# Kernel optimization log

Hardware: AMD Instinct MI355X
Metric: run time of the kernel (lower is better)

Reference implementation:

```python
import jax, jax.numpy as jnp
import numpy as np

B, T_PRIOR, N_FEAT = 8192, 168, 11
DEC_FEAT, HID, T_DEC = 7, 64, 48

def setup_inputs() -> dict:
    key = jax.random.key(0)
    ks = jax.random.split(key, 12)
    s = 1.0 / np.sqrt(HID)
    def u(k, shape):
        return jax.random.uniform(k, shape, jnp.float32, -s, s)
    return {
        "prior": jax.random.normal(ks[0], (B, T_PRIOR, N_FEAT), jnp.float32),
        "teacher_seq": jax.random.normal(ks[1], (B, T_DEC, DEC_FEAT), jnp.float32),
        "enc_Wih": u(ks[2], (3 * HID, N_FEAT)),
        "enc_Whh": u(ks[3], (3 * HID, HID)),
        "enc_bih": u(ks[4], (3 * HID,)),
        "enc_bhh": u(ks[5], (3 * HID,)),
        "dec_Wih": u(ks[6], (3 * HID, DEC_FEAT)),
        "dec_Whh": u(ks[7], (3 * HID, HID)),
        "dec_bih": u(ks[8], (3 * HID,)),
        "dec_bhh": u(ks[9], (3 * HID,)),
        "fc_W": u(ks[10], (1, HID)),
        "fc_b": u(ks[11], (1,)),
    }

def _gru_cell(x, h, Wih, Whh, bih, bhh):
    # PyTorch GRU gate math, gate order (r, z, n)
    gi = x @ Wih.T + bih            # [B, 3H]
    gh = h @ Whh.T + bhh            # [B, 3H]
    i_r, i_z, i_n = jnp.split(gi, 3, axis=-1)
    h_r, h_z, h_n = jnp.split(gh, 3, axis=-1)
    r = jax.nn.sigmoid(i_r + h_r)
    z = jax.nn.sigmoid(i_z + h_z)
    n = jnp.tanh(i_n + r * h_n)
    return (1.0 - z) * n + z * h

def reference(prior, teacher_seq, enc_Wih, enc_Whh, enc_bih, enc_bhh,
              dec_Wih, dec_Whh, dec_bih, dec_bhh, fc_W, fc_b):
    Bsz = prior.shape[0]
    h0 = jnp.zeros((Bsz, HID), prior.dtype)

    # ---- encoder: run GRU over prior, keep final hidden state ----
    def enc_step(h, x_t):
        return _gru_cell(x_t, h, enc_Wih, enc_Whh, enc_bih, enc_bhh), None
    h_enc, _ = jax.lax.scan(enc_step, h0, jnp.swapaxes(prior, 0, 1))

    # teacher features for step i+1, padded with zeros for the unused last step
    tn = jnp.concatenate(
        [teacher_seq[:, 1:, :], jnp.zeros_like(teacher_seq[:, :1, :])], axis=1)

    def dec_step(carry, tn_t):
        h, x = carry
        h = _gru_cell(x, h, dec_Wih, dec_Whh, dec_bih, dec_bhh)
        pred = h @ fc_W.T + fc_b                      # [B, 1]
        next_x = jnp.concatenate(
            [tn_t[:, 0:4], pred, tn_t[:, 5:7]], axis=-1)  # [B, 7]
        return (h, next_x), pred

    x0 = teacher_seq[:, 0, 0:7]
    (_, _), preds = jax.lax.scan(dec_step, (h_enc, x0), jnp.swapaxes(tn, 0, 1))
    # preds: [T_DEC, B, 1] -> [B, T_DEC]
    return jnp.swapaxes(preds[:, :, 0], 0, 1)
```

## Files before the change

kernel.cpp:

```cpp
#include <hip/hip_runtime.h>
#include <hip/hip_bf16.h>

#define T_PRIOR 168
#define N_FEAT 11
#define DEC_FEAT 7
#define T_DEC 48
#define BATCH 8192
#define XROWU 136
#define ROWB (XROWU*2)
#define BUFB (16*ROWB)

typedef __attribute__((ext_vector_type(8))) short short8;
typedef __attribute__((ext_vector_type(4))) float f32x4;
typedef __attribute__((ext_vector_type(4))) int i32x4;

#define MFMA __builtin_amdgcn_mfma_f32_16x16x32_bf16
#define L2E 1.4426950408889634f

static __device__ __forceinline__ unsigned fbits(float f){union{float f;unsigned u;}v;v.f=f;return v.u;}
static __device__ __forceinline__ unsigned short bf16rne(float f){
    unsigned x=fbits(f);
    return (unsigned short)((x+0x7fffu+((x>>16)&1u))>>16);
}
static __device__ __forceinline__ float sigm2(float xs){
    return __builtin_amdgcn_rcpf(1.0f + __builtin_amdgcn_exp2f(-xs));
}
static __device__ __forceinline__ float tanh2(float ys){
    return fmaf(2.0f, __builtin_amdgcn_rcpf(1.0f + __builtin_amdgcn_exp2f(-ys)), -1.0f);
}
static __device__ __forceinline__ short8 s8(i32x4 v){union{i32x4 i;short8 s;}q;q.i=v;return q.s;}
static __device__ __forceinline__ unsigned pk2bf(float a, float b){
    __hip_bfloat162 p = __float22bfloat162_rn(make_float2(a, b));
    union { __hip_bfloat162 h; unsigned u; } cv; cv.h = p; return cv.u;
}

__global__ __launch_bounds__(256) __attribute__((amdgpu_waves_per_eu(2,2)))
void gru_mfma(const float* __restrict__ prior, const float* __restrict__ teacher,
              const float* __restrict__ eWih, const float* __restrict__ eWhh,
              const float* __restrict__ eBih, const float* __restrict__ eBhh,
              const float* __restrict__ dWih, const float* __restrict__ dWhh,
              const float* __restrict__ dBih, const float* __restrict__ dBhh,
              const float* __restrict__ fcW, const float* __restrict__ fcB,
              float* __restrict__ out)
{
    __shared__ __align__(16) unsigned short sH[2][1024];
    __shared__ __align__(16) unsigned short sX[2*16*XROWU];
    __shared__ __align__(16) float sPartial[2][16][4];

    const int tid  = (int)threadIdx.x;
    const int lane = tid & 63;
    const int u    = tid >> 6;
    const int c    = lane & 15;
    const int g    = lane >> 4;
    const int row0 = (int)blockIdx.x * 16;

    const unsigned cs = ((unsigned)(c & 7)) << 4;
    const unsigned rbA0 = (unsigned)(c*128) + (((unsigned)(g*16)) ^ cs);
    const unsigned rbA1 = (unsigned)(c*128) + (((unsigned)(64 + g*16)) ^ cs);
    unsigned pubOff[4];
#pragma unroll
    for (int q = 0; q < 4; ++q) {
        int r = g*4 + q;
        pubOff[q] = (unsigned)(r*128) + (((unsigned)(32*u + 2*c)) ^ (((unsigned)(r&7))<<4));
    }

    const unsigned xRowB = (unsigned)(c*ROWB);
    const unsigned xE_off = (g < 2) ? (unsigned)(g*16) : 256u;
    const unsigned xE_mul = (g < 2) ? 32u : 0u;
    const unsigned xD_off = (g == 0) ? 0u : 256u;
    const unsigned xD_mul = (g == 0) ? 32u : 0u;
    char* sXB = (char*)sX;

    const int srow = tid >> 4, sli = tid & 15;
    char* sXwr = sXB + srow*ROWB;
    int offE[6], offD[4];
#pragma unroll
    for (int n = 0; n < 6; ++n) { int k = sli + 16*n; offE[n] = ((k/11)*16 + (k%11))*2; }
#pragma unroll
    for (int n = 0; n < 4; ++n) { int k = sli + 16*n; offD[n] = ((k/7)*16 + (k%7))*2; }
    const float* gP = prior   + (size_t)(row0 + srow)*(T_PRIOR*N_FEAT) + sli;
    const float* gT = teacher + (size_t)(row0 + srow)*(T_DEC*DEC_FEAT) + sli;

    short8 BHH[3][2], BIH[3];
    f32x4 bR4, bZ4, bH4, bI4;
    auto loadPhase = [&](const float* Wih, const float* Whh,
                         const float* bih, const float* bhh, int kvalid) {
        const int rwb = u*16 + c;
#pragma unroll
        for (int gate = 0; gate < 3; ++gate) {
            const float gs = (gate == 2) ? (2.0f*L2E) : L2E;
            const int rw = gate*64 + rwb;
#pragma unroll
            for (int kt = 0; kt < 2; ++kt) {
                union { short8 v; unsigned short s[8]; } fh;
#pragma unroll
                for (int j = 0; j < 8; ++j) {
                    int kap = kt*32 + g*8 + j;
                    fh.s[j] = bf16rne(Whh[rw*64 + kap] * gs);
                }
                BHH[gate][kt] = fh.v;
            }
            union { short8 v; unsigned short s[8]; } fi;
#pragma unroll
            for (int j = 0; j < 8; ++j) {
                int k = g*8 + j;
                fi.s[j] = (k < kvalid) ? bf16rne(Wih[rw*kvalid + k] * gs) : (unsigned short)0;
            }
            BIH[gate] = fi.v;
        }
        const int un = u*16 + c;
        float vR = (bih[un] + bhh[un]) * L2E;
        float vZ = (bih[64+un] + bhh[64+un]) * L2E;
        float vI = bih[128+un] * (2.0f*L2E);
        float vH = bhh[128+un] * (2.0f*L2E);
        bR4 = (f32x4){vR,vR,vR,vR};
        bZ4 = (f32x4){vZ,vZ,vZ,vZ};
        bH4 = (f32x4){vH,vH,vH,vH};
        bI4 = (f32x4){vI,vI,vI,vI};
    };

    float h[4] = {0.0f, 0.0f, 0.0f, 0.0f};

    auto gates_publish = [&](int p, f32x4 R, f32x4 Z, f32x4 Hh, f32x4 I) {
        char* hw = (char*)&sH[p^1][0];
        float hn[4];
#pragma unroll
        for (int q = 0; q < 4; ++q) {
            float rr = sigm2(R[q]);
            float zz = sigm2(Z[q]);
            float nn = tanh2(fmaf(rr, Hh[q], I[q]));
            hn[q] = nn + zz*(h[q] - nn);
            h[q] = hn[q];
        }
        unsigned w01 = pk2bf(hn[0], hn[1]);
        unsigned w23 = pk2bf(hn[2], hn[3]);
        *(unsigned short*)(hw + pubOff[0]) = (unsigned short)(w01 & 0xffffu);
        *(unsigned short*)(hw + pubOff[1]) = (unsigned short)(w01 >> 16);
        *(unsigned short*)(hw + pubOff[2]) = (unsigned short)(w23 & 0xffffu);
        *(unsigned short*)(hw + pubOff[3]) = (unsigned short)(w23 >> 16);
    };

    f32x4 xR, xZ, xI;
    auto xpart = [&](short8 xf) {
        xR = MFMA(xf, BIH[0], bR4, 0,0,0);
        xZ = MFMA(xf, BIH[1], bZ4, 0,0,0);
        xI = MFMA(xf, BIH[2], bI4, 0,0,0);
    };

    auto hh_step = [&](int p) {
        const char* hb = (const char*)&sH[p][0];
        short8 a0 = *(const short8*)(hb + rbA0);
        short8 a1 = *(const short8*)(hb + rbA1);
        __builtin_amdgcn_s_setprio(1);
        f32x4 R = MFMA(a0, BHH[0][0], xR, 0,0,0);
        R = MFMA(a1, BHH[0][1], R, 0,0,0);
        f32x4 Z = MFMA(a0, BHH[1][0], xZ, 0,0,0);
        Z = MFMA(a1, BHH[1][1], Z, 0,0,0);
        f32x4 Hh = MFMA(a0, BHH[2][0], bH4, 0,0,0);
        Hh = MFMA(a1, BHH[2][1], Hh, 0,0,0);
        __builtin_amdgcn_s_setprio(0);
        gates_publish(p, R, Z, Hh, xI);
    };

    auto gru_step = [&](int p, short8 xf) {
        const char* hb = (const char*)&sH[p][0];
        short8 a0 = *(const short8*)(hb + rbA0);
        short8 a1 = *(const short8*)(hb + rbA1);
        f32x4 R = MFMA(a0, BHH[0][0], bR4, 0,0,0);
        R = MFMA(a1, BHH[0][1], R, 0,0,0);
        R = MFMA(xf, BIH[0],    R, 0,0,0);
        f32x4 Z = MFMA(a0, BHH[1][0], bZ4, 0,0,0);
        Z = MFMA(a1, BHH[1][1], Z, 0,0,0);
        Z = MFMA(xf, BIH[1],    Z, 0,0,0);
        f32x4 Hh = MFMA(a0, BHH[2][0], bH4, 0,0,0);
        Hh = MFMA(a1, BHH[2][1], Hh, 0,0,0);
        f32x4 I = MFMA(xf, BIH[2], bI4, 0,0,0);
        gates_publish(p, R, Z, Hh, I);
    };

    {
        unsigned* z0 = (unsigned*)&sH[0][0];
#pragma unroll
        for (int it = 0; it < 2; ++it) z0[tid + 256*it] = 0u;
    }
#pragma unroll
    for (int it = 0; it < 6; ++it) {
        int e = tid + 256*it;
        int b = e / 768, rem = e % 768;
        int idx;
        if (rem < 640) {
            int r = rem / 40, q2 = rem % 40;
            idx = b*(16*XROWU) + r*XROWU + (q2/5)*16 + 11 + q2%5;
        } else {
            int rem2 = rem - 640;
            idx = b*(16*XROWU) + (rem2 >> 3)*XROWU + 128 + (rem2 & 7);
        }
        sX[idx] = 0;
    }
    loadPhase(eWih, eWhh, eBih, eBhh, N_FEAT);
    {
        float sv[6];
#pragma unroll
        for (int n = 0; n < 5; ++n) sv[n] = gP[16*n];
        sv[5] = (sli < 8) ? gP[80] : 0.0f;
#pragma unroll
        for (int n = 0; n < 5; ++n) *(unsigned short*)(sXwr + offE[n]) = bf16rne(sv[n]);
        if (sli < 8) *(unsigned short*)(sXwr + offE[5]) = bf16rne(sv[5]);
    }
    __syncthreads();
    {
        short8 xf0 = *(const short8*)(sXB + (xRowB + xE_off));
        xpart(xf0);
    }

    for (int ch = 0; ch < 21; ++ch) {
        const unsigned wbo = (unsigned)(((ch + 1) & 1) * BUFB);
        const bool st = (ch < 20);
        float sv[6];
#pragma unroll
        for (int s = 0; s < 8; ++s) {
            const int t = ch*8 + s;
            __syncthreads();
            if (s == 0 && st) {
                const float* sp = gP + 88*(ch+1);
#pragma unroll
                for (int n = 0; n < 5; ++n) sv[n] = sp[16*n];
                sv[5] = (sli < 8) ? sp[80] : 0.0f;
            }
            hh_step(t & 1);
            if (s == 1 && st) {
#pragma unroll
                for (int n = 0; n < 5; ++n) *(unsigned short*)(sXwr + wbo + offE[n]) = bf16rne(sv[n]);
                if (sli < 8) *(unsigned short*)(sXwr + wbo + offE[5]) = bf16rne(sv[5]);
            }
            if (t < T_PRIOR - 1) {
                const int tn = t + 1;
                const unsigned nbo = (unsigned)(((tn >> 3) & 1) * BUFB);
                short8 xf = *(const short8*)(sXB + (nbo + xRowB + xE_off + (unsigned)(tn & 7)*xE_mul));
                xpart(xf);
            }
        }
    }

    __syncthreads();
    loadPhase(dWih, dWhh, dBih, dBhh, DEC_FEAT);
    const float fwc = fcW[u*16 + c];
    const float fb  = fcB[0];
#pragma unroll
    for (int it = 0; it < 9; ++it) {
        int e = tid + 256*it;
        int b = e / 1152, rem = e % 1152;
        int r = rem / 72, q2 = rem % 72;
        sX[b*(16*XROWU) + r*XROWU + (q2/9)*16 + 7 + q2%9] = 0;
    }
    {
        float sv[4];
#pragma unroll
        for (int n = 0; n < 3; ++n) sv[n] = gT[16*n];
        sv[3] = (sli < 8) ? gT[48] : 0.0f;
#pragma unroll
        for (int n = 0; n < 3; ++n) *(unsigned short*)(sXwr + offD[n]) = bf16rne(sv[n]);
        if (sli < 8) *(unsigned short*)(sXwr + offD[3]) = bf16rne(sv[3]);
    }

    for (int ch = 0; ch < 6; ++ch) {
        const unsigned bo  = (unsigned)((ch & 1) * BUFB);
        const unsigned wbo = (unsigned)(((ch + 1) & 1) * BUFB);
        const bool st = (ch < 5);
        float sv[4];
#pragma unroll
        for (int s = 0; s < 8; ++s) {
            const int i = ch*8 + s;
            __syncthreads();
            if (s == 0 && st) {
                const float* sp = gT + 56*(ch+1);
#pragma unroll
                for (int n = 0; n < 3; ++n) sv[n] = sp[16*n];
                sv[3] = (sli < 8) ? sp[48] : 0.0f;
            }
            const bool hasPred = (s > 0) || (ch > 0);
            i32x4 xi = *(const i32x4*)(sXB + (bo + xRowB + xD_off + (unsigned)s*xD_mul));
            if (hasPred) {
                f32x4 pp = *(const f32x4*)&sPartial[(s & 1) ^ 1][c][0];
                float pred = pp[0] + pp[1] + pp[2] + pp[3] + fb;
                if (g == 0)
                    xi[2] = (int)(((unsigned)xi[2] & 0xffff0000u) | (unsigned)bf16rne(pred));
                if (u == 0 && g == 0)
                    out[(size_t)(row0 + c)*T_DEC + (i - 1)] = pred;
            }
            gru_step(s & 1, s8(xi));
#pragma unroll
            for (int q = 0; q < 4; ++q) {
                float v = h[q] * fwc;
                v += __shfl_xor(v, 1, 64);
                v += __shfl_xor(v, 2, 64);
                v += __shfl_xor(v, 4, 64);
                v += __shfl_xor(v, 8, 64);
                if (c == 0) sPartial[s & 1][g*4 + q][u] = v;
            }
            if (s == 1 && st) {
#pragma unroll
                for (int n = 0; n < 3; ++n) *(unsigned short*)(sXwr + wbo + offD[n]) = bf16rne(sv[n]);
                if (sli < 8) *(unsigned short*)(sXwr + wbo + offD[3]) = bf16rne(sv[3]);
            }
        }
    }
    __syncthreads();
    if (u == 0 && g == 0) {
        f32x4 pp = *(const f32x4*)&sPartial[1][c][0];
        float pred = pp[0] + pp[1] + pp[2] + pp[3] + fb;
        out[(size_t)(row0 + c)*T_DEC + (T_DEC - 1)] = pred;
    }
}

extern "C" void kernel_launch(void* const* d_in, const int* in_sizes, int n_in,
                              void* d_out, int out_size, void* d_ws, size_t ws_size,
                              hipStream_t stream)
{
    const float* prior   = (const float*)d_in[0];
    const float* teacher = (const float*)d_in[1];
    const float* eWih    = (const float*)d_in[2];
    const float* eWhh    = (const float*)d_in[3];
    const float* eBih    = (const float*)d_in[4];
    const float* eBhh    = (const float*)d_in[5];
    const float* dWih    = (const float*)d_in[6];
    const float* dWhh    = (const float*)d_in[7];
    const float* dBih    = (const float*)d_in[8];
    const float* dBhh    = (const float*)d_in[9];
    const float* fcW     = (const float*)d_in[10];
    const float* fcB     = (const float*)d_in[11];
    float* out = (float*)d_out;

    dim3 grid(BATCH / 16);
    dim3 block(256);
    hipLaunchKernelGGL(gru_mfma, grid, block, 0, stream,
                       prior, teacher, eWih, eWhh, eBih, eBhh,
                       dWih, dWhh, dBih, dBhh, fcW, fcB, out);
}
```

Before: 142.6 us.

## Split GRU hidden-state K dimension across two wave groups with LDS exchange

Doubles the block to 512 threads and splits the 64-wide hidden reduction (K) between two wave groups. Each group computes half of the Whh MFMAs and half the input projections, then exchanges partial accumulators through shared memory so each group finishes gate math for half the rows. This shortens the serial per-step MFMA chain and spreads the gate math across more waves. In exchange it adds a second barrier per timestep, LDS exchange traffic, and a single hidden buffer instead of a double buffer.

Result: slower. 511.0 us (+258.3%).

```diff
diff --git a/kernel.cpp b/kernel.cpp
--- a/kernel.cpp
+++ b/kernel.cpp
@@ -12,6 +12,7 @@
 
 typedef __attribute__((ext_vector_type(8))) short short8;
 typedef __attribute__((ext_vector_type(4))) float f32x4;
+typedef __attribute__((ext_vector_type(2))) float f32x2;
 typedef __attribute__((ext_vector_type(4))) int i32x4;
 
 #define MFMA __builtin_amdgcn_mfma_f32_16x16x32_bf16
@@ -34,33 +35,35 @@
     union { __hip_bfloat162 h; unsigned u; } cv; cv.h = p; return cv.u;
 }
 
-__global__ __launch_bounds__(256) __attribute__((amdgpu_waves_per_eu(2,2)))
-void gru_mfma(const float* __restrict__ prior, const float* __restrict__ teacher,
-              const float* __restrict__ eWih, const float* __restrict__ eWhh,
-              const float* __restrict__ eBih, const float* __restrict__ eBhh,
-              const float* __restrict__ dWih, const float* __restrict__ dWhh,
-              const float* __restrict__ dBih, const float* __restrict__ dBhh,
-              const float* __restrict__ fcW, const float* __restrict__ fcB,
-              float* __restrict__ out)
+__global__ __launch_bounds__(512)
+void gru_ks(const float* __restrict__ prior, const float* __restrict__ teacher,
+            const float* __restrict__ eWih, const float* __restrict__ eWhh,
+            const float* __restrict__ eBih, const float* __restrict__ eBhh,
+            const float* __restrict__ dWih, const float* __restrict__ dWhh,
+            const float* __restrict__ dBih, const float* __restrict__ dBhh,
+            const float* __restrict__ fcW, const float* __restrict__ fcB,
+            float* __restrict__ out)
 {
-    __shared__ __align__(16) unsigned short sH[2][1024];
+    __shared__ __align__(16) unsigned short sH[1024];
+    __shared__ __align__(16) float sXch[2][4][4][128];
     __shared__ __align__(16) unsigned short sX[2*16*XROWU];
     __shared__ __align__(16) float sPartial[2][16][4];
 
     const int tid  = (int)threadIdx.x;
     const int lane = tid & 63;
-    const int u    = tid >> 6;
+    const int w    = tid >> 6;
+    const int u    = w & 3;
+    const int sW   = __builtin_amdgcn_readfirstlane(w >> 2);
     const int c    = lane & 15;
     const int g    = lane >> 4;
     const int row0 = (int)blockIdx.x * 16;
 
     const unsigned cs = ((unsigned)(c & 7)) << 4;
-    const unsigned rbA0 = (unsigned)(c*128) + (((unsigned)(g*16)) ^ cs);
-    const unsigned rbA1 = (unsigned)(c*128) + (((unsigned)(64 + g*16)) ^ cs);
-    unsigned pubOff[4];
-#pragma unroll
-    for (int q = 0; q < 4; ++q) {
-        int r = g*4 + q;
+    const unsigned rbA = (unsigned)(c*128) + (((unsigned)(sW*64 + g*16)) ^ cs);
+    unsigned pubOff[2];
+#pragma unroll
+    for (int q = 0; q < 2; ++q) {
+        int r = g*4 + sW*2 + q;
         pubOff[q] = (unsigned)(r*128) + (((unsigned)(32*u + 2*c)) ^ (((unsigned)(r&7))<<4));
     }
 
@@ -71,7 +74,11 @@
     const unsigned xD_mul = (g == 0) ? 32u : 0u;
     char* sXB = (char*)sX;
 
-    const int srow = tid >> 4, sli = tid & 15;
+    float* xw = &sXch[sW][u][0][0] + lane*2;
+    const float* xr = &sXch[sW^1][u][0][0] + lane*2;
+
+    const bool stager = (tid < 256);
+    const int srow = (tid & 255) >> 4, sli = tid & 15;
     char* sXwr = sXB + srow*ROWB;
     int offE[6], offD[4];
 #pragma unroll
@@ -81,111 +88,135 @@
     const float* gP = prior   + (size_t)(row0 + srow)*(T_PRIOR*N_FEAT) + sli;
     const float* gT = teacher + (size_t)(row0 + srow)*(T_DEC*DEC_FEAT) + sli;
 
-    short8 BHH[3][2], BIH[3];
-    f32x4 bR4, bZ4, bH4, bI4;
+    short8 BHH[3];
+    short8 BIx[2];
+    float bR, bZ, bH, bI;
     auto loadPhase = [&](const float* Wih, const float* Whh,
-                         const float* bih, const float* bhh, int kvalid) {
+                         const float* bih, const float* bhh, int kv) {
         const int rwb = u*16 + c;
 #pragma unroll
         for (int gate = 0; gate < 3; ++gate) {
             const float gs = (gate == 2) ? (2.0f*L2E) : L2E;
             const int rw = gate*64 + rwb;
-#pragma unroll
-            for (int kt = 0; kt < 2; ++kt) {
-                union { short8 v; unsigned short s[8]; } fh;
-#pragma unroll
-                for (int j = 0; j < 8; ++j) {
-                    int kap = kt*32 + g*8 + j;
-                    fh.s[j] = bf16rne(Whh[rw*64 + kap] * gs);
-                }
-                BHH[gate][kt] = fh.v;
-            }
+            union { short8 v; unsigned short s[8]; } fh;
+#pragma unroll
+            for (int j = 0; j < 8; ++j)
+                fh.s[j] = bf16rne(Whh[rw*64 + sW*32 + g*8 + j] * gs);
+            BHH[gate] = fh.v;
+        }
+        auto mkBI = [&](int gate) -> short8 {
+            const float gs = (gate == 2) ? (2.0f*L2E) : L2E;
+            const int rw = gate*64 + rwb;
             union { short8 v; unsigned short s[8]; } fi;
 #pragma unroll
             for (int j = 0; j < 8; ++j) {
                 int k = g*8 + j;
-                fi.s[j] = (k < kvalid) ? bf16rne(Wih[rw*kvalid + k] * gs) : (unsigned short)0;
-            }
-            BIH[gate] = fi.v;
-        }
+                fi.s[j] = (k < kv) ? bf16rne(Wih[rw*kv + k] * gs) : (unsigned short)0;
+            }
+            return fi.v;
+        };
+        if (sW == 0) { BIx[0] = mkBI(2); }
+        else         { BIx[0] = mkBI(0); BIx[1] = mkBI(1); }
         const int un = u*16 + c;
-        float vR = (bih[un] + bhh[un]) * L2E;
-        float vZ = (bih[64+un] + bhh[64+un]) * L2E;
-        float vI = bih[128+un] * (2.0f*L2E);
-        float vH = bhh[128+un] * (2.0f*L2E);
-        bR4 = (f32x4){vR,vR,vR,vR};
-        bZ4 = (f32x4){vZ,vZ,vZ,vZ};
-        bH4 = (f32x4){vH,vH,vH,vH};
-        bI4 = (f32x4){vI,vI,vI,vI};
-    };
-
-    float h[4] = {0.0f, 0.0f, 0.0f, 0.0f};
-
-    auto gates_publish = [&](int p, f32x4 R, f32x4 Z, f32x4 Hh, f32x4 I) {
-        char* hw = (char*)&sH[p^1][0];
-        float hn[4];
-#pragma unroll
-        for (int q = 0; q < 4; ++q) {
-            float rr = sigm2(R[q]);
-            float zz = sigm2(Z[q]);
-            float nn = tanh2(fmaf(rr, Hh[q], I[q]));
-            hn[q] = nn + zz*(h[q] - nn);
-            h[q] = hn[q];
-        }
-        unsigned w01 = pk2bf(hn[0], hn[1]);
-        unsigned w23 = pk2bf(hn[2], hn[3]);
-        *(unsigned short*)(hw + pubOff[0]) = (unsigned short)(w01 & 0xffffu);
-        *(unsigned short*)(hw + pubOff[1]) = (unsigned short)(w01 >> 16);
-        *(unsigned short*)(hw + pubOff[2]) = (unsigned short)(w23 & 0xffffu);
-        *(unsigned short*)(hw + pubOff[3]) = (unsigned short)(w23 >> 16);
-    };
-
-    f32x4 xR, xZ, xI;
-    auto xpart = [&](short8 xf) {
-        xR = MFMA(xf, BIH[0], bR4, 0,0,0);
-        xZ = MFMA(xf, BIH[1], bZ4, 0,0,0);
-        xI = MFMA(xf, BIH[2], bI4, 0,0,0);
-    };
-
-    auto hh_step = [&](int p) {
-        const char* hb = (const char*)&sH[p][0];
-        short8 a0 = *(const short8*)(hb + rbA0);
-        short8 a1 = *(const short8*)(hb + rbA1);
+        bR = (bih[un] + bhh[un]) * L2E;
+        bZ = (bih[64+un] + bhh[64+un]) * L2E;
+        bI = bih[128+un] * (2.0f*L2E);
+        bH = bhh[128+un] * (2.0f*L2E);
+    };
+
+    const f32x4 z4 = (f32x4){0.0f, 0.0f, 0.0f, 0.0f};
+    f32x4 xpR, xpZ, xpI;
+    f32x4 aR, aZ, aH, aI;
+    float h0 = 0.0f, h1 = 0.0f;
+    float fwc = 0.0f, fb = 0.0f;
+
+    auto xpartE = [&](short8 xf) {
+        if (sW == 0) { xpI = MFMA(xf, BIx[0], z4, 0,0,0); }
+        else         { xpR = MFMA(xf, BIx[0], z4, 0,0,0);
+                       xpZ = MFMA(xf, BIx[1], z4, 0,0,0); }
+    };
+
+    auto xch_write = [&]() {
+        if (sW == 0) {
+            *(f32x2*)(xw +   0) = (f32x2){aR[2], aR[3]};
+            *(f32x2*)(xw + 128) = (f32x2){aZ[2], aZ[3]};
+            *(f32x2*)(xw + 256) = (f32x2){aH[2], aH[3]};
+            *(f32x2*)(xw + 384) = (f32x2){aI[2], aI[3]};
+        } else {
+            *(f32x2*)(xw +   0) = (f32x2){aR[0], aR[1]};
+            *(f32x2*)(xw + 128) = (f32x2){aZ[0], aZ[1]};
+            *(f32x2*)(xw + 256) = (f32x2){aH[0], aH[1]};
+        }
+    };
+
+    auto phase1E = [&]() {
+        short8 a = *(const short8*)((const char*)sH + rbA);
         __builtin_amdgcn_s_setprio(1);
-        f32x4 R = MFMA(a0, BHH[0][0], xR, 0,0,0);
-        R = MFMA(a1, BHH[0][1], R, 0,0,0);
-        f32x4 Z = MFMA(a0, BHH[1][0], xZ, 0,0,0);
-        Z = MFMA(a1, BHH[1][1], Z, 0,0,0);
-        f32x4 Hh = MFMA(a0, BHH[2][0], bH4, 0,0,0);
-        Hh = MFMA(a1, BHH[2][1], Hh, 0,0,0);
+        if (sW == 0) {
+            aR = MFMA(a, BHH[0], z4, 0,0,0);
+            aZ = MFMA(a, BHH[1], z4, 0,0,0);
+            aH = MFMA(a, BHH[2], z4, 0,0,0);
+            aI = xpI;
+        } else {
+            aR = MFMA(a, BHH[0], xpR, 0,0,0);
+            aZ = MFMA(a, BHH[1], xpZ, 0,0,0);
+            aH = MFMA(a, BHH[2], z4, 0,0,0);
+        }
         __builtin_amdgcn_s_setprio(0);
-        gates_publish(p, R, Z, Hh, xI);
-    };
-
-    auto gru_step = [&](int p, short8 xf) {
-        const char* hb = (const char*)&sH[p][0];
-        short8 a0 = *(const short8*)(hb + rbA0);
-        short8 a1 = *(const short8*)(hb + rbA1);
-        f32x4 R = MFMA(a0, BHH[0][0], bR4, 0,0,0);
-        R = MFMA(a1, BHH[0][1], R, 0,0,0);
-        R = MFMA(xf, BIH[0],    R, 0,0,0);
-        f32x4 Z = MFMA(a0, BHH[1][0], bZ4, 0,0,0);
-        Z = MFMA(a1, BHH[1][1], Z, 0,0,0);
-        Z = MFMA(xf, BIH[1],    Z, 0,0,0);
-        f32x4 Hh = MFMA(a0, BHH[2][0], bH4, 0,0,0);
-        Hh = MFMA(a1, BHH[2][1], Hh, 0,0,0);
-        f32x4 I = MFMA(xf, BIH[2], bI4, 0,0,0);
-        gates_publish(p, R, Z, Hh, I);
-    };
-
-    {
-        unsigned* z0 = (unsigned*)&sH[0][0];
-#pragma unroll
-        for (int it = 0; it < 2; ++it) z0[tid + 256*it] = 0u;
-    }
-#pragma unroll
-    for (int it = 0; it < 6; ++it) {
-        int e = tid + 256*it;
+        xch_write();
+    };
+
+    auto phase1D = [&](short8 xf) {
+        short8 a = *(const short8*)((const char*)sH + rbA);
+        __builtin_amdgcn_s_setprio(1);
+        if (sW == 0) {
+            aR = MFMA(a, BHH[0], z4, 0,0,0);
+            aZ = MFMA(a, BHH[1], z4, 0,0,0);
+            aH = MFMA(a, BHH[2], z4, 0,0,0);
+            aI = MFMA(xf, BIx[0], z4, 0,0,0);
+        } else {
+            aR = MFMA(a, BHH[0], z4, 0,0,0);
+            aR = MFMA(xf, BIx[0], aR, 0,0,0);
+            aZ = MFMA(a, BHH[1], z4, 0,0,0);
+            aZ = MFMA(xf, BIx[1], aZ, 0,0,0);
+            aH = MFMA(a, BHH[2], z4, 0,0,0);
+        }
+        __builtin_amdgcn_s_setprio(0);
+        xch_write();
+    };
+
+    auto phase2 = [&]() {
+        f32x2 pR = *(const f32x2*)(xr +   0);
+        f32x2 pZ = *(const f32x2*)(xr + 128);
+        f32x2 pH = *(const f32x2*)(xr + 256);
+        float Rt0, Rt1, Zt0, Zt1, Ht0, Ht1, It0, It1;
+        if (sW == 0) {
+            Rt0 = aR[0]+pR[0]+bR; Rt1 = aR[1]+pR[1]+bR;
+            Zt0 = aZ[0]+pZ[0]+bZ; Zt1 = aZ[1]+pZ[1]+bZ;
+            Ht0 = aH[0]+pH[0]+bH; Ht1 = aH[1]+pH[1]+bH;
+            It0 = aI[0]+bI;       It1 = aI[1]+bI;
+        } else {
+            f32x2 pI = *(const f32x2*)(xr + 384);
+            Rt0 = aR[2]+pR[0]+bR; Rt1 = aR[3]+pR[1]+bR;
+            Zt0 = aZ[2]+pZ[0]+bZ; Zt1 = aZ[3]+pZ[1]+bZ;
+            Ht0 = aH[2]+pH[0]+bH; Ht1 = aH[3]+pH[1]+bH;
+            It0 = pI[0]+bI;       It1 = pI[1]+bI;
+        }
+        float rr0 = sigm2(Rt0), zz0 = sigm2(Zt0);
+        float nn0 = tanh2(fmaf(rr0, Ht0, It0));
+        h0 = nn0 + zz0*(h0 - nn0);
+        float rr1 = sigm2(Rt1), zz1 = sigm2(Zt1);
+        float nn1 = tanh2(fmaf(rr1, Ht1, It1));
+        h1 = nn1 + zz1*(h1 - nn1);
+        unsigned w01 = pk2bf(h0, h1);
+        *(unsigned short*)((char*)sH + pubOff[0]) = (unsigned short)(w01 & 0xffffu);
+        *(unsigned short*)((char*)sH + pubOff[1]) = (unsigned short)(w01 >> 16);
+    };
+
+    if (tid < 512) ((unsigned*)sH)[tid] = 0u;
+#pragma unroll
+    for (int it = 0; it < 3; ++it) {
+        int e = tid + 512*it;
         int b = e / 768, rem = e % 768;
         int idx;
         if (rem < 640) {
@@ -198,7 +229,7 @@
         sX[idx] = 0;
     }
     loadPhase(eWih, eWhh, eBih, eBhh, N_FEAT);
-    {
+    if (stager) {
         float sv[6];
 #pragma unroll
         for (int n = 0; n < 5; ++n) sv[n] = gP[16*n];
@@ -210,7 +241,7 @@
     __syncthreads();
     {
         short8 xf0 = *(const short8*)(sXB + (xRowB + xE_off));
-        xpart(xf0);
+        xpartE(xf0);
     }
 
     for (int ch = 0; ch < 21; ++ch) {
@@ -221,14 +252,16 @@
         for (int s = 0; s < 8; ++s) {
             const int t = ch*8 + s;
             __syncthreads();
-            if (s == 0 && st) {
+            if (s == 0 && st && stager) {
                 const float* sp = gP + 88*(ch+1);
 #pragma unroll
                 for (int n = 0; n < 5; ++n) sv[n] = sp[16*n];
                 sv[5] = (sli < 8) ? sp[80] : 0.0f;
             }
-            hh_step(t & 1);
-            if (s == 1 && st) {
+            phase1E();
+            __syncthreads();
+            phase2();
+            if (s == 1 && st && stager) {
 #pragma unroll
                 for (int n = 0; n < 5; ++n) *(unsigned short*)(sXwr + wbo + offE[n]) = bf16rne(sv[n]);
                 if (sli < 8) *(unsigned short*)(sXwr + wbo + offE[5]) = bf16rne(sv[5]);
@@ -237,23 +270,25 @@
                 const int tn = t + 1;
                 const unsigned nbo = (unsigned)(((tn >> 3) & 1) * BUFB);
                 short8 xf = *(const short8*)(sXB + (nbo + xRowB + xE_off + (unsigned)(tn & 7)*xE_mul));
-                xpart(xf);
+                xpartE(xf);
             }
         }
     }
 
     __syncthreads();
     loadPhase(dWih, dWhh, dBih, dBhh, DEC_FEAT);
-    const float fwc = fcW[u*16 + c];
-    const float fb  = fcB[0];
-#pragma unroll
-    for (int it = 0; it < 9; ++it) {
-        int e = tid + 256*it;
-        int b = e / 1152, rem = e % 1152;
-        int r = rem / 72, q2 = rem % 72;
-        sX[b*(16*XROWU) + r*XROWU + (q2/9)*16 + 7 + q2%9] = 0;
-    }
-    {
+    fwc = fcW[u*16 + c];
+    fb  = fcB[0];
+#pragma unroll
+    for (int it = 0; it < 5; ++it) {
+        int e = tid + 512*it;
+        if (e < 2304) {
+            int b = e / 1152, rem = e % 1152;
+            int r = rem / 72, q2 = rem % 72;
+            sX[b*(16*XROWU) + r*XROWU + (q2/9)*16 + 7 + q2%9] = 0;
+        }
+    }
+    if (stager) {
         float sv[4];
 #pragma unroll
         for (int n = 0; n < 3; ++n) sv[n] = gT[16*n];
@@ -272,33 +307,37 @@
         for (int s = 0; s < 8; ++s) {
             const int i = ch*8 + s;
             __syncthreads();
-            if (s == 0 && st) {
+            if (s == 0 && st && stager) {
                 const float* sp = gT + 56*(ch+1);
 #pragma unroll
                 for (int n = 0; n < 3; ++n) sv[n] = sp[16*n];
                 sv[3] = (sli < 8) ? sp[48] : 0.0f;
             }
-            const bool hasPred = (s > 0) || (ch > 0);
+            const bool hasPred = (i > 0);
             i32x4 xi = *(const i32x4*)(sXB + (bo + xRowB + xD_off + (unsigned)s*xD_mul));
             if (hasPred) {
                 f32x4 pp = *(const f32x4*)&sPartial[(s & 1) ^ 1][c][0];
                 float pred = pp[0] + pp[1] + pp[2] + pp[3] + fb;
                 if (g == 0)
                     xi[2] = (int)(((unsigned)xi[2] & 0xffff0000u) | (unsigned)bf16rne(pred));
-                if (u == 0 && g == 0)
+                if (w == 0 && g == 0)
                     out[(size_t)(row0 + c)*T_DEC + (i - 1)] = pred;
             }
-            gru_step(s & 1, s8(xi));
-#pragma unroll
-            for (int q = 0; q < 4; ++q) {
-                float v = h[q] * fwc;
-                v += __shfl_xor(v, 1, 64);
-                v += __shfl_xor(v, 2, 64);
-                v += __shfl_xor(v, 4, 64);
-                v += __shfl_xor(v, 8, 64);
-                if (c == 0) sPartial[s & 1][g*4 + q][u] = v;
-            }
-            if (s == 1 && st) {
+            phase1D(s8(xi));
+            __syncthreads();
+            phase2();
+            {
+                float v0 = h0 * fwc, v1 = h1 * fwc;
+                v0 += __shfl_xor(v0, 1, 64); v1 += __shfl_xor(v1, 1, 64);
+                v0 += __shfl_xor(v0, 2, 64); v1 += __shfl_xor(v1, 2, 64);
+                v0 += __shfl_xor(v0, 4, 64); v1 += __shfl_xor(v1, 4, 64);
+                v0 += __shfl_xor(v0, 8, 64); v1 += __shfl_xor(v1, 8, 64);
+                if (c == 0) {
+                    sPartial[s & 1][g*4 + sW*2 + 0][u] = v0;
+                    sPartial[s & 1][g*4 + sW*2 + 1][u] = v1;
+                }
+            }
+            if (s == 1 && st && stager) {
 #pragma unroll
                 for (int n = 0; n < 3; ++n) *(unsigned short*)(sXwr + wbo + offD[n]) = bf16rne(sv[n]);
                 if (sli < 8) *(unsigned short*)(sXwr + wbo + offD[3]) = bf16rne(sv[3]);
@@ -306,7 +345,7 @@
         }
     }
     __syncthreads();
-    if (u == 0 && g == 0) {
+    if (w == 0 && g == 0) {
         f32x4 pp = *(const f32x4*)&sPartial[1][c][0];
         float pred = pp[0] + pp[1] + pp[2] + pp[3] + fb;
         out[(size_t)(row0 + c)*T_DEC + (T_DEC - 1)] = pred;
@@ -332,8 +371,8 @@
     float* out = (float*)d_out;
 
     dim3 grid(BATCH / 16);
-    dim3 block(256);
-    hipLaunchKernelGGL(gru_mfma, grid, block, 0, stream,
+    dim3 block(512);
+    hipLaunchKernelGGL(gru_ks, grid, block, 0, stream,
                        prior, teacher, eWih, eWhh, eBih, eBhh,
                        dWih, dWhh, dBih, dBhh, fcW, fcB, out);
 }
```
